# Kernel optimization log

Measured on AMD Instinct MI355X. Metric: run time of the kernel, lower is better.

Reference implementation:

```python
import jax, jax.numpy as jnp
import numpy as np

D_MODEL = 512
N_HEADS = 8
D_HEAD = D_MODEL // N_HEADS
N_LAYERS = 6
VOCAB = 32000
B, S = 4, 1024
EPS = 1e-5


def positional_encoding(length, d_model):
    # matches get_positional_encoding_table: pos * (1/10000**(i/d)), sin on even i, cos on odd i
    inv = 1.0 / (10000.0 ** (jnp.arange(d_model, dtype=jnp.float32) / d_model))
    ang = jnp.arange(length, dtype=jnp.float32)[:, None] * inv[None, :]  # [S, D]
    pe = jnp.where(jnp.arange(d_model) % 2 == 0, jnp.sin(ang), jnp.cos(ang))
    return pe


def layer_norm(x, g, b):
    m = jnp.mean(x, axis=-1, keepdims=True)
    v = jnp.mean((x - m) ** 2, axis=-1, keepdims=True)
    return (x - m) * jax.lax.rsqrt(v + EPS) * g + b


def setup_inputs() -> dict:
    key = jax.random.key(0)
    ks = jax.random.split(key, 9)
    sc = 0.02
    return {
        "tokens": jax.random.randint(ks[0], (B, S), 0, VOCAB),
        "emb": jax.random.normal(ks[1], (VOCAB, D_MODEL), jnp.float32) * sc,
        "Wq": jax.random.normal(ks[2], (N_LAYERS, D_MODEL, D_MODEL), jnp.float32) * sc,
        "bq": jnp.zeros((N_LAYERS, D_MODEL), jnp.float32),
        "Wk": jax.random.normal(ks[3], (N_LAYERS, D_MODEL, D_MODEL), jnp.float32) * sc,
        "bk": jnp.zeros((N_LAYERS, D_MODEL), jnp.float32),
        "Wv": jax.random.normal(ks[4], (N_LAYERS, D_MODEL, D_MODEL), jnp.float32) * sc,
        "bv": jnp.zeros((N_LAYERS, D_MODEL), jnp.float32),
        "Wo": jax.random.normal(ks[5], (N_LAYERS, D_MODEL, D_MODEL), jnp.float32) * sc,
        "bo": jnp.zeros((N_LAYERS, D_MODEL), jnp.float32),
        "W1": jax.random.normal(ks[6], (N_LAYERS, D_MODEL, 4 * D_MODEL), jnp.float32) * sc,
        "b1": jnp.zeros((N_LAYERS, 4 * D_MODEL), jnp.float32),
        "W2": jax.random.normal(ks[7], (N_LAYERS, 4 * D_MODEL, D_MODEL), jnp.float32) * sc,
        "b2": jnp.zeros((N_LAYERS, D_MODEL), jnp.float32),
        "ln_g": jnp.ones((N_LAYERS, D_MODEL), jnp.float32),
        "ln_b": jnp.zeros((N_LAYERS, D_MODEL), jnp.float32),
    }


def encoder_layer(x, Wq, bq, Wk, bk, Wv, bv, Wo, bo, W1, b1, W2, b2, g, b):
    bsz = x.shape[0]
    q = (x @ Wq + bq).reshape(bsz, -1, N_HEADS, D_HEAD).transpose(0, 2, 1, 3)  # [B,h,S,dk]
    k = (x @ Wk + bk).reshape(bsz, -1, N_HEADS, D_HEAD).transpose(0, 2, 1, 3)
    v = (x @ Wv + bv).reshape(bsz, -1, N_HEADS, D_HEAD).transpose(0, 2, 1, 3)
    scores = jnp.einsum('bhqd,bhkd->bhqk', q, k) / (D_HEAD ** 0.5)
    w = jax.nn.softmax(scores, axis=-1)
    attn = jnp.einsum('bhqk,bhkd->bhqd', w, v)  # [B,h,S,dv]
    # faithful to source bug: .view(B,-1,h*dv) WITHOUT transposing heads back
    attn = attn.reshape(bsz, -1, N_HEADS * D_HEAD)  # [B,S,D] with heads/seq interleaved
    x = layer_norm(x + (attn @ Wo + bo), g, b)
    ffn = jnp.maximum(x @ W1 + b1, 0.0) @ W2 + b2
    x = layer_norm(x + ffn, g, b)  # same (shared) LayerNorm params, as in source
    return x


def reference(tokens, emb, Wq, bq, Wk, bk, Wv, bv, Wo, bo, W1, b1, W2, b2, ln_g, ln_b):
    x = emb[tokens]  # [B,S,D]
    x = x + positional_encoding(x.shape[1], D_MODEL)
    for i in range(N_LAYERS):
        x = encoder_layer(x, Wq[i], bq[i], Wk[i], bk[i], Wv[i], bv[i], Wo[i], bo[i],
                          W1[i], b1[i], W2[i], b2[i], ln_g[i], ln_b[i])
    return x
```

## Files before the change

### kernel.cpp

```cpp
#include <hip/hip_runtime.h>
#include <hip/hip_bf16.h>
#include <math.h>

typedef unsigned short ushort_t;
typedef __attribute__((ext_vector_type(8))) short bfrag_t;
typedef __attribute__((ext_vector_type(4))) float facc_t;

#define D_MODEL 512
#define NH 8
#define DH 64
#define NL 6
#define BB 4
#define SS 1024
#define ROWS (BB*SS)
#define DFF 2048

__device__ inline ushort_t f2bf(float f) {
    __hip_bfloat16 h = __float2bfloat16(f);
    return *(ushort_t*)&h;
}
__device__ inline float bf2f(ushort_t u) {
    unsigned int x = ((unsigned int)u) << 16;
    union { unsigned int i; float f; } c; c.i = x;
    return c.f;
}
__device__ inline void gload_lds16(const void* g, void* l) {
    __builtin_amdgcn_global_load_lds((const __attribute__((address_space(1))) unsigned int*)g,
                                     (__attribute__((address_space(3))) unsigned int*)l, 16, 0, 0);
}

__global__ __launch_bounds__(256) void embed_pe(const int* __restrict__ tok,
                                                const float* __restrict__ emb,
                                                float* __restrict__ x,
                                                ushort_t* __restrict__ xbf) {
    int row = blockIdx.x;
    int s = row & (SS - 1);
    int t = tok[row];
    const float* e = emb + (size_t)t * D_MODEL;
    for (int i = threadIdx.x; i < D_MODEL; i += 256) {
        float freq = __expf(-9.210340371976184f * ((float)i / (float)D_MODEL));
        float ang = (float)s * freq;
        float pe = (i & 1) ? cosf(ang) : sinf(ang);
        float v = e[i] + pe;
        x[(size_t)row * D_MODEL + i] = v;
        xbf[(size_t)row * D_MODEL + i] = f2bf(v);
    }
}

__global__ __launch_bounds__(256) void prep_weights(const float* __restrict__ Wq,
                                                    const float* __restrict__ Wk,
                                                    const float* __restrict__ Wv,
                                                    const float* __restrict__ Wo,
                                                    const float* __restrict__ W1,
                                                    const float* __restrict__ W2,
                                                    int layer, ushort_t* __restrict__ wlay) {
    __shared__ float tile[32][33];
    int z = blockIdx.z;
    const float* src; ushort_t* dst; int K, N;
    size_t o512 = (size_t)layer * 512 * 512;
    size_t o1M  = (size_t)layer * 512 * 2048;
    switch (z) {
        case 0: src = Wq + o512; dst = wlay;               K = 512;  N = 512;  break;
        case 1: src = Wk + o512; dst = wlay + 262144;      K = 512;  N = 512;  break;
        case 2: src = Wv + o512; dst = wlay + 524288;      K = 512;  N = 512;  break;
        case 3: src = Wo + o512; dst = wlay + 786432;      K = 512;  N = 512;  break;
        case 4: src = W1 + o1M;  dst = wlay + 1048576;     K = 512;  N = 2048; break;
        default:src = W2 + o1M;  dst = wlay + 2097152;     K = 2048; N = 512;  break;
    }
    int n0 = blockIdx.x * 32, k0 = blockIdx.y * 32;
    if (n0 >= N || k0 >= K) return;
    int tx = threadIdx.x & 31, ty = threadIdx.x >> 5;
    #pragma unroll
    for (int i = 0; i < 4; i++)
        tile[ty + i * 8][tx] = src[(size_t)(k0 + ty + i * 8) * N + n0 + tx];
    __syncthreads();
    #pragma unroll
    for (int i = 0; i < 4; i++)
        dst[(size_t)(n0 + ty + i * 8) * K + k0 + tx] = f2bf(tile[tx][ty + i * 8]);
}

__global__ __launch_bounds__(256) void concat_bias(const float* __restrict__ bq,
                                                   const float* __restrict__ bk,
                                                   const float* __restrict__ bv,
                                                   float* __restrict__ bqkv) {
    int l = blockIdx.x;
    for (int i = threadIdx.x; i < 1536; i += 256) {
        float v = (i < 512) ? bq[l * 512 + i]
                : (i < 1024) ? bk[l * 512 + i - 512]
                : bv[l * 512 + i - 1024];
        bqkv[l * 1536 + i] = v;
    }
}

__global__ __launch_bounds__(256) void gemm_mfma(const ushort_t* __restrict__ A,
                                                 const ushort_t* __restrict__ Bt,
                                                 const float* __restrict__ bias,
                                                 float* __restrict__ Cf,
                                                 ushort_t* __restrict__ Cb,
                                                 int N, int K, int relu) {
    __shared__ ushort_t lA[128 * 64];
    __shared__ ushort_t lB[128 * 64];

    const int tid = threadIdx.x;
    const int w = tid >> 6, lane = tid & 63;
    const int wr = w & 1, wc = w >> 1;
    const int lane16 = lane & 15, quad = lane >> 4;
    const int row0 = blockIdx.y * 128, col0 = blockIdx.x * 128;

    facc_t acc[4][4];
    #pragma unroll
    for (int i = 0; i < 4; i++)
        #pragma unroll
        for (int j = 0; j < 4; j++)
            acc[i][j] = (facc_t){0.f, 0.f, 0.f, 0.f};

    for (int k0 = 0; k0 < K; k0 += 64) {
        __syncthreads();
        #pragma unroll
        for (int i = 0; i < 4; i++) {
            int g = w * 256 + i * 64 + lane;
            int r = g >> 3, p = g & 7;
            int q = p ^ (r & 7);
            gload_lds16(A + (size_t)(row0 + r) * K + k0 + q * 8, lA + (size_t)g * 8);
            gload_lds16(Bt + (size_t)(col0 + r) * K + k0 + q * 8, lB + (size_t)g * 8);
        }
        __syncthreads();

        #pragma unroll
        for (int kk = 0; kk < 2; kk++) {
            bfrag_t af[4], bfg[4];
            #pragma unroll
            for (int t = 0; t < 4; t++) {
                int m = wr * 64 + t * 16 + lane16;
                int q = kk * 4 + quad;
                af[t] = *(const bfrag_t*)(lA + ((size_t)m * 8 + (q ^ (m & 7))) * 8);
                int n = wc * 64 + t * 16 + lane16;
                bfg[t] = *(const bfrag_t*)(lB + ((size_t)n * 8 + (q ^ (n & 7))) * 8);
            }
            #pragma unroll
            for (int ti = 0; ti < 4; ti++)
                #pragma unroll
                for (int tj = 0; tj < 4; tj++)
                    acc[ti][tj] = __builtin_amdgcn_mfma_f32_16x16x32_bf16(
                        af[ti], bfg[tj], acc[ti][tj], 0, 0, 0);
        }
    }

    float bv_[4];
    #pragma unroll
    for (int tj = 0; tj < 4; tj++)
        bv_[tj] = bias[col0 + wc * 64 + tj * 16 + lane16];

    #pragma unroll
    for (int ti = 0; ti < 4; ti++) {
        int grow_base = row0 + wr * 64 + ti * 16 + quad * 4;
        #pragma unroll
        for (int tj = 0; tj < 4; tj++) {
            int gcol = col0 + wc * 64 + tj * 16 + lane16;
            #pragma unroll
            for (int rr = 0; rr < 4; rr++) {
                float v = acc[ti][tj][rr] + bv_[tj];
                if (relu) v = fmaxf(v, 0.f);
                size_t idx = (size_t)(grow_base + rr) * N + gcol;
                if (Cf) Cf[idx] = v;
                if (Cb) Cb[idx] = f2bf(v);
            }
        }
    }
}

__global__ __launch_bounds__(256) void gemm_mfma64(const ushort_t* __restrict__ A,
                                                   const ushort_t* __restrict__ Bt,
                                                   const float* __restrict__ bias,
                                                   float* __restrict__ Cf,
                                                   ushort_t* __restrict__ Cb,
                                                   int N, int K, int relu) {
    __shared__ ushort_t lA[64 * 64];
    __shared__ ushort_t lB[64 * 64];

    const int tid = threadIdx.x;
    const int w = tid >> 6, lane = tid & 63;
    const int wr = w & 1, wc = w >> 1;
    const int lane16 = lane & 15, quad = lane >> 4;
    const int row0 = blockIdx.y * 64, col0 = blockIdx.x * 64;

    facc_t acc[2][2];
    #pragma unroll
    for (int i = 0; i < 2; i++)
        #pragma unroll
        for (int j = 0; j < 2; j++)
            acc[i][j] = (facc_t){0.f, 0.f, 0.f, 0.f};

    for (int k0 = 0; k0 < K; k0 += 64) {
        __syncthreads();
        #pragma unroll
        for (int i = 0; i < 2; i++) {
            int g = w * 128 + i * 64 + lane;
            int r = g >> 3, p = g & 7;
            int q = p ^ (r & 7);
            gload_lds16(A + (size_t)(row0 + r) * K + k0 + q * 8, lA + (size_t)g * 8);
            gload_lds16(Bt + (size_t)(col0 + r) * K + k0 + q * 8, lB + (size_t)g * 8);
        }
        __syncthreads();

        #pragma unroll
        for (int kk = 0; kk < 2; kk++) {
            bfrag_t af[2], bfg[2];
            #pragma unroll
            for (int t = 0; t < 2; t++) {
                int m = wr * 32 + t * 16 + lane16;
                int q = kk * 4 + quad;
                af[t] = *(const bfrag_t*)(lA + ((size_t)m * 8 + (q ^ (m & 7))) * 8);
                int n = wc * 32 + t * 16 + lane16;
                bfg[t] = *(const bfrag_t*)(lB + ((size_t)n * 8 + (q ^ (n & 7))) * 8);
            }
            #pragma unroll
            for (int ti = 0; ti < 2; ti++)
                #pragma unroll
                for (int tj = 0; tj < 2; tj++)
                    acc[ti][tj] = __builtin_amdgcn_mfma_f32_16x16x32_bf16(
                        af[ti], bfg[tj], acc[ti][tj], 0, 0, 0);
        }
    }

    float bv_[2];
    #pragma unroll
    for (int tj = 0; tj < 2; tj++)
        bv_[tj] = bias[col0 + wc * 32 + tj * 16 + lane16];

    #pragma unroll
    for (int ti = 0; ti < 2; ti++) {
        int grow_base = row0 + wr * 32 + ti * 16 + quad * 4;
        #pragma unroll
        for (int tj = 0; tj < 2; tj++) {
            int gcol = col0 + wc * 32 + tj * 16 + lane16;
            #pragma unroll
            for (int rr = 0; rr < 4; rr++) {
                float v = acc[ti][tj][rr] + bv_[tj];
                if (relu) v = fmaxf(v, 0.f);
                size_t idx = (size_t)(grow_base + rr) * N + gcol;
                if (Cf) Cf[idx] = v;
                if (Cb) Cb[idx] = f2bf(v);
            }
        }
    }
}

__global__ __launch_bounds__(128) void attn_mfma_split(const ushort_t* __restrict__ qkv,
                                                       ushort_t* __restrict__ Yp,
                                                       float2* __restrict__ mlp) {
    __shared__ __align__(16) ushort_t lK[4096];
    __shared__ __align__(16) ushort_t lVT[4096];
    __shared__ __align__(16) ushort_t lP[2048];

    const int tid = threadIdx.x;
    const int w = tid >> 6, lane = tid & 63;
    const int lane16 = lane & 15, quad = lane >> 4;
    const int qt = blockIdx.x, h = blockIdx.y;
    const int b = blockIdx.z >> 1, kh = blockIdx.z & 1;
    const int kt0 = kh * 8;

    const ushort_t* Qrow = qkv + (size_t)(b * SS + qt * 32 + w * 16 + lane16) * 1536 + h * 64;
    bfrag_t qa[2];
    #pragma unroll
    for (int ks = 0; ks < 2; ks++)
        qa[ks] = *(const bfrag_t*)(Qrow + ks * 32 + quad * 8);

    facc_t O[4];
    #pragma unroll
    for (int t = 0; t < 4; t++) O[t] = (facc_t){0.f, 0.f, 0.f, 0.f};
    float mrow[4] = {-INFINITY, -INFINITY, -INFINITY, -INFINITY};
    float lrow[4] = {0.f, 0.f, 0.f, 0.f};

    const int vkey = tid & 63;
    const int vdg  = tid >> 6;
    const int vk8 = vkey >> 3, vj = vkey & 7;

    const float LOG2E = 1.4426950408889634f;
    const float SC = 0.125f * 1.4426950408889634f;

    auto stageK = [&](int kt) {
        #pragma unroll
        for (int i = 0; i < 4; i++) {
            int g = i * 128 + tid;
            int r = g >> 3, p = g & 7;
            int q = p ^ (r & 7);
            gload_lds16(qkv + (size_t)(b * SS + kt * 64 + r) * 1536 + h * 64 + 512 + q * 8,
                        lK + (size_t)g * 8);
        }
    };
    auto loadV = [&](int kt, ushort_t* vs) {
        const ushort_t* vsrc = qkv + (size_t)(b * SS + kt * 64 + vkey) * 1536
                               + h * 64 + 1024 + vdg * 32;
        #pragma unroll
        for (int i4 = 0; i4 < 4; i4++)
            *(uint4*)(vs + i4 * 8) = *(const uint4*)(vsrc + i4 * 8);
    };
    auto writeV = [&](const ushort_t* vs) {
        #pragma unroll
        for (int e = 0; e < 32; e++) {
            int n = vdg * 32 + e;
            lVT[(size_t)(n * 8 + (vk8 ^ (n & 7))) * 8 + vj] = vs[e];
        }
    };

    ushort_t vcur[32];
    loadV(kt0, vcur);

    for (int kt = kt0; kt < kt0 + 8; kt++) {
        stageK(kt);
        writeV(vcur);
        __syncthreads();

        if (kt < kt0 + 7) loadV(kt + 1, vcur);

        facc_t sf[4];
        #pragma unroll
        for (int t = 0; t < 4; t++) sf[t] = (facc_t){0.f, 0.f, 0.f, 0.f};
        #pragma unroll
        for (int ks = 0; ks < 2; ks++) {
            #pragma unroll
            for (int t = 0; t < 4; t++) {
                int row = t * 16 + lane16;
                int q = ks * 4 + quad;
                bfrag_t kf = *(const bfrag_t*)(lK + ((size_t)row * 8 + (q ^ (row & 7))) * 8);
                sf[t] = __builtin_amdgcn_mfma_f32_16x16x32_bf16(qa[ks], kf, sf[t], 0, 0, 0);
            }
        }

        float mt_[4];
        #pragma unroll
        for (int r = 0; r < 4; r++)
            mt_[r] = fmaxf(fmaxf(sf[0][r], sf[1][r]), fmaxf(sf[2][r], sf[3][r])) * 0.125f;
        #pragma unroll
        for (int off = 1; off < 16; off <<= 1)
            #pragma unroll
            for (int r = 0; r < 4; r++)
                mt_[r] = fmaxf(mt_[r], __shfl_xor(mt_[r], off));

        bool small = (mt_[0] <= mrow[0] + 8.f) && (mt_[1] <= mrow[1] + 8.f)
                  && (mt_[2] <= mrow[2] + 8.f) && (mt_[3] <= mrow[3] + 8.f);
        if (!__all(small)) {
            #pragma unroll
            for (int r = 0; r < 4; r++) {
                float mn = fmaxf(mrow[r], mt_[r]);
                float al = __builtin_amdgcn_exp2f((mrow[r] - mn) * LOG2E);
                mrow[r] = mn;
                lrow[r] *= al;
                O[0][r] *= al; O[1][r] *= al; O[2][r] *= al; O[3][r] *= al;
            }
        }
        float mC[4];
        #pragma unroll
        for (int r = 0; r < 4; r++) mC[r] = mrow[r] * LOG2E;

        float ps[4] = {0.f, 0.f, 0.f, 0.f};
        ushort_t* Pw = lP + w * 1024;
        #pragma unroll
        for (int t = 0; t < 4; t++) {
            int k8 = t * 2 + (lane16 >> 3);
            int j = lane16 & 7;
            #pragma unroll
            for (int r = 0; r < 4; r++) {
                float p = __builtin_amdgcn_exp2f(fmaf(sf[t][r], SC, -mC[r]));
                ps[r] += p;
                int row = quad * 4 + r;
                Pw[(size_t)(row * 8 + (k8 ^ (row & 7))) * 8 + j] = f2bf(p);
            }
        }
        #pragma unroll
        for (int off = 1; off < 16; off <<= 1)
            #pragma unroll
            for (int r = 0; r < 4; r++)
                ps[r] += __shfl_xor(ps[r], off);
        #pragma unroll
        for (int r = 0; r < 4; r++)
            lrow[r] += ps[r];

        #pragma unroll
        for (int ks = 0; ks < 2; ks++) {
            int q = ks * 4 + quad;
            bfrag_t pf = *(const bfrag_t*)(Pw + ((size_t)lane16 * 8 + (q ^ (lane16 & 7))) * 8);
            #pragma unroll
            for (int t = 0; t < 4; t++) {
                int n = t * 16 + lane16;
                bfrag_t vf = *(const bfrag_t*)(lVT + ((size_t)n * 8 + (q ^ (n & 7))) * 8);
                O[t] = __builtin_amdgcn_mfma_f32_16x16x32_bf16(pf, vf, O[t], 0, 0, 0);
            }
        }
        __syncthreads();
    }

    size_t rbase = ((size_t)(kh * BB + b) * NH + h) * SS + qt * 32 + w * 16 + quad * 4;
    #pragma unroll
    for (int r = 0; r < 4; r++) {
        float inv = 1.f / lrow[r];
        #pragma unroll
        for (int t = 0; t < 4; t++)
            Yp[(rbase + r) * DH + t * 16 + lane16] = f2bf(O[t][r] * inv);
        if (lane16 == 0)
            mlp[rbase + r] = make_float2(mrow[r], lrow[r]);
    }
}

__global__ __launch_bounds__(256) void attn_combine(const ushort_t* __restrict__ Yp,
                                                    const float2* __restrict__ mlp,
                                                    ushort_t* __restrict__ ab) {
    const float LOG2E = 1.4426950408889634f;
    int rid = blockIdx.x * 32 + (threadIdx.x >> 3);
    int d0 = (threadIdx.x & 7) * 8;
    float2 ml0 = mlp[rid];
    float2 ml1 = mlp[32768 + rid];
    float m = fmaxf(ml0.x, ml1.x);
    float a0 = __builtin_amdgcn_exp2f((ml0.x - m) * LOG2E) * ml0.y;
    float a1 = __builtin_amdgcn_exp2f((ml1.x - m) * LOG2E) * ml1.y;
    float inv = 1.f / (a0 + a1);
    a0 *= inv; a1 *= inv;
    uint4 u0 = *(const uint4*)(Yp + (size_t)rid * DH + d0);
    uint4 u1 = *(const uint4*)(Yp + (size_t)32768 * DH + (size_t)rid * DH + d0);
    const ushort_t* p0 = (const ushort_t*)&u0;
    const ushort_t* p1 = (const ushort_t*)&u1;
    ushort_t o[8];
    #pragma unroll
    for (int e = 0; e < 8; e++)
        o[e] = f2bf(a0 * bf2f(p0[e]) + a1 * bf2f(p1[e]));
    *(uint4*)(ab + (size_t)rid * DH + d0) = *(uint4*)o;
}

__global__ __launch_bounds__(256) void add_ln(const float* __restrict__ x,
                                              const float* __restrict__ delta,
                                              const float* __restrict__ g,
                                              const float* __restrict__ bparm,
                                              float* __restrict__ outf,
                                              ushort_t* __restrict__ outb) {
    __shared__ float red[2][4];
    int row = blockIdx.x;
    int t = threadIdx.x;
    const float* xr = x + (size_t)row * D_MODEL;
    const float* dr = delta + (size_t)row * D_MODEL;
    float v0 = xr[t] + dr[t];
    float v1 = xr[t + 256] + dr[t + 256];
    float s = v0 + v1;
    float ss = v0 * v0 + v1 * v1;
    #pragma unroll
    for (int off = 1; off < 64; off <<= 1) {
        s  += __shfl_xor(s, off);
        ss += __shfl_xor(ss, off);
    }
    int lane = t & 63, wid = t >> 6;
    if (lane == 0) { red[0][wid] = s; red[1][wid] = ss; }
    __syncthreads();
    s  = red[0][0] + red[0][1] + red[0][2] + red[0][3];
    ss = red[1][0] + red[1][1] + red[1][2] + red[1][3];
    float mean = s * (1.f / D_MODEL);
    float var = ss * (1.f / D_MODEL) - mean * mean;
    float rinv = rsqrtf(var + 1e-5f);
    float o0 = (v0 - mean) * rinv * g[t]       + bparm[t];
    float o1 = (v1 - mean) * rinv * g[t + 256] + bparm[t + 256];
    float* orow = outf + (size_t)row * D_MODEL;
    orow[t] = o0; orow[t + 256] = o1;
    ushort_t* brow = outb + (size_t)row * D_MODEL;
    brow[t] = f2bf(o0); brow[t + 256] = f2bf(o1);
}

extern "C" void kernel_launch(void* const* d_in, const int* in_sizes, int n_in,
                              void* d_out, int out_size, void* d_ws, size_t ws_size,
                              hipStream_t stream) {
    const int* tokens = (const int*)d_in[0];
    const float* emb = (const float*)d_in[1];
    const float* Wq = (const float*)d_in[2];  const float* bq = (const float*)d_in[3];
    const float* Wk = (const float*)d_in[4];  const float* bk = (const float*)d_in[5];
    const float* Wv = (const float*)d_in[6];  const float* bv = (const float*)d_in[7];
    const float* Wo = (const float*)d_in[8];  const float* bo = (const float*)d_in[9];
    const float* W1 = (const float*)d_in[10]; const float* b1 = (const float*)d_in[11];
    const float* W2 = (const float*)d_in[12]; const float* b2 = (const float*)d_in[13];
    const float* lng = (const float*)d_in[14]; const float* lnb = (const float*)d_in[15];

    char* base = (char*)d_ws;
    ushort_t* wlay = (ushort_t*)(base);
    float*    bqkv = (float*)   (base + 6291456);
    float*    x    = (float*)   (base + 6328320);
    ushort_t* xbf  = (ushort_t*)(base + 14716928);
    float*    tmp  = (float*)   (base + 18911232);
    ushort_t* qkv  = (ushort_t*)(base + 27299840);
    ushort_t* ab   = (ushort_t*)(base + 39882752);
    ushort_t* mid  = qkv;

    ushort_t* Yp  = (ushort_t*)tmp;
    float2*   mlp = (float2*)xbf;

    ushort_t* wqkv_t = wlay;
    ushort_t* wo_t   = wlay + 786432;
    ushort_t* w1_t   = wlay + 1048576;
    ushort_t* w2_t   = wlay + 2097152;

    concat_bias<<<NL, 256, 0, stream>>>(bq, bk, bv, bqkv);
    embed_pe<<<ROWS, 256, 0, stream>>>(tokens, emb, x, xbf);

    for (int l = 0; l < NL; l++) {
        prep_weights<<<dim3(64, 64, 6), 256, 0, stream>>>(Wq, Wk, Wv, Wo, W1, W2, l, wlay);

        gemm_mfma<<<dim3(12, 32), 256, 0, stream>>>(xbf, wqkv_t, bqkv + l * 1536,
                                                    nullptr, qkv, 1536, 512, 0);
        attn_mfma_split<<<dim3(32, NH, BB * 2), 128, 0, stream>>>(qkv, Yp, mlp);
        attn_combine<<<1024, 256, 0, stream>>>(Yp, mlp, ab);

        gemm_mfma64<<<dim3(8, 64), 256, 0, stream>>>(ab, wo_t, bo + l * D_MODEL,
                                                     tmp, nullptr, 512, 512, 0);
        add_ln<<<ROWS, 256, 0, stream>>>(x, tmp, lng + l * D_MODEL, lnb + l * D_MODEL,
                                         x, xbf);

        gemm_mfma<<<dim3(16, 32), 256, 0, stream>>>(xbf, w1_t, b1 + l * DFF,
                                                    nullptr, mid, 2048, 512, 1);
        gemm_mfma64<<<dim3(8, 64), 256, 0, stream>>>(mid, w2_t, b2 + l * D_MODEL,
                                                     tmp, nullptr, 512, 2048, 0);
        float* lnout = (l == NL - 1) ? (float*)d_out : x;
        add_ln<<<ROWS, 256, 0, stream>>>(x, tmp, lng + l * D_MODEL, lnb + l * D_MODEL,
                                         lnout, xbf);
    }
}
```

Before: 973.2 us.

## Double-buffer V tiles and widen attention blocks to four waves

The attention kernel now uses 256 threads per block covering 64 query rows, so each staged K/V tile is reused by twice as many queries. The V transpose buffer is double-buffered, and the next K tile is staged right after the QK MFMA, overlapping global loads with softmax and PV compute. This cuts K/V traffic per query and hides load latency. In exchange it halves the grid size and uses more LDS per block, which may lower occupancy.

```diff
diff --git a/kernel.cpp b/kernel.cpp
--- a/kernel.cpp
+++ b/kernel.cpp
@@ -246,12 +246,12 @@
     }
 }
 
-__global__ __launch_bounds__(128) void attn_mfma_split(const ushort_t* __restrict__ qkv,
+__global__ __launch_bounds__(256) void attn_mfma_split(const ushort_t* __restrict__ qkv,
                                                        ushort_t* __restrict__ Yp,
                                                        float2* __restrict__ mlp) {
     __shared__ __align__(16) ushort_t lK[4096];
-    __shared__ __align__(16) ushort_t lVT[4096];
-    __shared__ __align__(16) ushort_t lP[2048];
+    __shared__ __align__(16) ushort_t lVT[2][4096];
+    __shared__ __align__(16) ushort_t lP[4096];
 
     const int tid = threadIdx.x;
     const int w = tid >> 6, lane = tid & 63;
@@ -260,7 +260,7 @@
     const int b = blockIdx.z >> 1, kh = blockIdx.z & 1;
     const int kt0 = kh * 8;
 
-    const ushort_t* Qrow = qkv + (size_t)(b * SS + qt * 32 + w * 16 + lane16) * 1536 + h * 64;
+    const ushort_t* Qrow = qkv + (size_t)(b * SS + qt * 64 + w * 16 + lane16) * 1536 + h * 64;
     bfrag_t qa[2];
     #pragma unroll
     for (int ks = 0; ks < 2; ks++)
@@ -281,8 +281,8 @@
 
     auto stageK = [&](int kt) {
         #pragma unroll
-        for (int i = 0; i < 4; i++) {
-            int g = i * 128 + tid;
+        for (int i = 0; i < 2; i++) {
+            int g = i * 256 + tid;
             int r = g >> 3, p = g & 7;
             int q = p ^ (r & 7);
             gload_lds16(qkv + (size_t)(b * SS + kt * 64 + r) * 1536 + h * 64 + 512 + q * 8,
@@ -291,28 +291,32 @@
     };
     auto loadV = [&](int kt, ushort_t* vs) {
         const ushort_t* vsrc = qkv + (size_t)(b * SS + kt * 64 + vkey) * 1536
-                               + h * 64 + 1024 + vdg * 32;
-        #pragma unroll
-        for (int i4 = 0; i4 < 4; i4++)
-            *(uint4*)(vs + i4 * 8) = *(const uint4*)(vsrc + i4 * 8);
+                               + h * 64 + 1024 + vdg * 16;
+        *(uint4*)(vs)     = *(const uint4*)(vsrc);
+        *(uint4*)(vs + 8) = *(const uint4*)(vsrc + 8);
     };
-    auto writeV = [&](const ushort_t* vs) {
-        #pragma unroll
-        for (int e = 0; e < 32; e++) {
-            int n = vdg * 32 + e;
-            lVT[(size_t)(n * 8 + (vk8 ^ (n & 7))) * 8 + vj] = vs[e];
+    auto writeV = [&](const ushort_t* vs, int buf) {
+        #pragma unroll
+        for (int e = 0; e < 16; e++) {
+            int n = vdg * 16 + e;
+            lVT[buf][(size_t)(n * 8 + (vk8 ^ (n & 7))) * 8 + vj] = vs[e];
         }
     };
 
-    ushort_t vcur[32];
-    loadV(kt0, vcur);
+    {
+        ushort_t v0[16];
+        stageK(kt0);
+        loadV(kt0, v0);
+        writeV(v0, 0);
+    }
+    __syncthreads();
 
     for (int kt = kt0; kt < kt0 + 8; kt++) {
-        stageK(kt);
-        writeV(vcur);
-        __syncthreads();
-
-        if (kt < kt0 + 7) loadV(kt + 1, vcur);
+        const int buf = (kt - kt0) & 1;
+        const bool more = (kt < kt0 + 7);
+
+        ushort_t vn[16];
+        if (more) loadV(kt + 1, vn);
 
         facc_t sf[4];
         #pragma unroll
@@ -326,6 +330,11 @@
                 bfrag_t kf = *(const bfrag_t*)(lK + ((size_t)row * 8 + (q ^ (row & 7))) * 8);
                 sf[t] = __builtin_amdgcn_mfma_f32_16x16x32_bf16(qa[ks], kf, sf[t], 0, 0, 0);
             }
+        }
+
+        if (more) {
+            __syncthreads();
+            stageK(kt + 1);
         }
 
         float mt_[4];
@@ -377,6 +386,8 @@
         for (int r = 0; r < 4; r++)
             lrow[r] += ps[r];
 
+        if (more) writeV(vn, buf ^ 1);
+
         #pragma unroll
         for (int ks = 0; ks < 2; ks++) {
             int q = ks * 4 + quad;
@@ -384,14 +395,15 @@
             #pragma unroll
             for (int t = 0; t < 4; t++) {
                 int n = t * 16 + lane16;
-                bfrag_t vf = *(const bfrag_t*)(lVT + ((size_t)n * 8 + (q ^ (n & 7))) * 8);
+                bfrag_t vf = *(const bfrag_t*)(&lVT[buf][((size_t)n * 8 + (q ^ (n & 7))) * 8]);
                 O[t] = __builtin_amdgcn_mfma_f32_16x16x32_bf16(pf, vf, O[t], 0, 0, 0);
             }
         }
+
         __syncthreads();
     }
 
-    size_t rbase = ((size_t)(kh * BB + b) * NH + h) * SS + qt * 32 + w * 16 + quad * 4;
+    size_t rbase = ((size_t)(kh * BB + b) * NH + h) * SS + qt * 64 + w * 16 + quad * 4;
     #pragma unroll
     for (int r = 0; r < 4; r++) {
         float inv = 1.f / lrow[r];
@@ -502,7 +514,7 @@
 
         gemm_mfma<<<dim3(12, 32), 256, 0, stream>>>(xbf, wqkv_t, bqkv + l * 1536,
                                                     nullptr, qkv, 1536, 512, 0);
-        attn_mfma_split<<<dim3(32, NH, BB * 2), 128, 0, stream>>>(qkv, Yp, mlp);
+        attn_mfma_split<<<dim3(16, NH, BB * 2), 256, 0, stream>>>(qkv, Yp, mlp);
         attn_combine<<<1024, 256, 0, stream>>>(Yp, mlp, ab);
 
         gemm_mfma64<<<dim3(8, 64), 256, 0, stream>>>(ab, wo_t, bo + l * D_MODEL,
```

After: 962.3 us. No clear change (-1.1%).
